# Kernel optimization log

Measured on AMD Instinct MI355X. Metric: run time of the kernel, lower is better.

Reference implementation:

```python
import jax, jax.numpy as jnp
from jax import lax
import numpy as np

V, K, T, E = 20000, 50, 50, 300   # vocab, topics, windows, rho_size
TH, EH, L, B = 800, 200, 3, 64    # t_hidden, eta_hidden, lstm layers, batch
DELTA = 0.005


def setup_inputs() -> dict:
    key = jax.random.key(0)
    ks = jax.random.split(key, 32)
    f32 = jnp.float32
    def nrm(i, shape, scale=1.0):
        return jax.random.normal(ks[i], shape, f32) * scale
    w = 0.02  # small init for linear weights so softplus/exp paths stay sane
    return {
        'bows': jax.random.uniform(ks[0], (B, V), f32),
        'normalized_bows': jax.random.uniform(ks[1], (B, V), f32),
        'times': jax.random.randint(ks[2], (B,), 0, T),
        'rnn_inp': jax.random.uniform(ks[3], (T, V), f32),
        'num_docs': 100000,
        'eps_alpha': nrm(4, (T, K, E)),
        'eps_eta': nrm(5, (T, K)),
        'eps_theta': nrm(6, (B, K)),
        'rho': nrm(7, (V, E), 0.1),
        'mu_q_alpha': nrm(8, (K, T, E), 0.1),
        'logsigma_q_alpha': nrm(9, (K, T, E), 0.1),
        'qtheta_W1': nrm(10, (TH, V + K), w), 'qtheta_b1': jnp.zeros((TH,), f32),
        'qtheta_W2': nrm(11, (TH, TH), w), 'qtheta_b2': jnp.zeros((TH,), f32),
        'mu_theta_W': nrm(12, (K, TH), w), 'mu_theta_b': jnp.zeros((K,), f32),
        'ls_theta_W': nrm(13, (K, TH), w), 'ls_theta_b': jnp.zeros((K,), f32),
        'eta_map_W': nrm(14, (EH, V), w), 'eta_map_b': jnp.zeros((EH,), f32),
        'lstm_Wih': nrm(15, (L, 4 * EH, EH), w), 'lstm_Whh': nrm(16, (L, 4 * EH, EH), w),
        'lstm_bih': jnp.zeros((L, 4 * EH), f32), 'lstm_bhh': jnp.zeros((L, 4 * EH), f32),
        'mu_eta_W': nrm(17, (K, EH + K), w), 'mu_eta_b': jnp.zeros((K,), f32),
        'ls_eta_W': nrm(18, (K, EH + K), w), 'ls_eta_b': jnp.zeros((K,), f32),
    }


def _kl(q_mu, q_ls, p_mu, p_ls):
    # KL(N(q_mu, e^{q_ls}) || N(p_mu, e^{p_ls})), summed over last dim (matches torch)
    return 0.5 * jnp.sum((jnp.exp(q_ls) + (q_mu - p_mu) ** 2) / (jnp.exp(p_ls) + 1e-6)
                         - 1.0 + p_ls - q_ls, axis=-1)


def _detm_forward(rho, mu_q_alpha, logsigma_q_alpha, qtheta_W1, qtheta_b1, qtheta_W2,
                  qtheta_b2, mu_theta_W, mu_theta_b, ls_theta_W, ls_theta_b, eta_map_W,
                  eta_map_b, lstm_Wih, lstm_Whh, lstm_bih, lstm_bhh, mu_eta_W, mu_eta_b,
                  ls_eta_W, ls_eta_b, bows, normalized_bows, rnn_inp, eps_alpha, eps_eta,
                  eps_theta, times):
    f32 = normalized_bows.dtype
    log_delta = jnp.log(jnp.asarray(DELTA, f32))
    zK = jnp.zeros((K,), f32)

    # ---- get_alpha (training): reparam is vectorizable; KL chains on alpha[t-1] ----
    mu_a = jnp.transpose(mu_q_alpha, (1, 0, 2))        # (T,K,E)
    ls_a = jnp.transpose(logsigma_q_alpha, (1, 0, 2))  # (T,K,E)
    alphas = mu_a + eps_alpha * jnp.exp(0.5 * ls_a)    # (T,K,E)
    kl_a0 = _kl(mu_a[0], ls_a[0], jnp.zeros_like(mu_a[0]), jnp.zeros_like(ls_a[0]))
    kl_at = _kl(mu_a[1:], ls_a[1:], alphas[:-1], log_delta)  # (T-1,K)
    kl_alpha = kl_a0.sum() + kl_at.sum()

    # ---- get_eta: q_eta_map -> 3-layer LSTM (batch 1) -> sequential eta chain ----
    x = rnn_inp @ eta_map_W.T + eta_map_b  # (T,EH)
    for l in range(L):
        Wih, Whh = lstm_Wih[l], lstm_Whh[l]
        bih, bhh = lstm_bih[l], lstm_bhh[l]
        def cell(carry, xt):
            h, c = carry
            g = Wih @ xt + bih + Whh @ h + bhh
            i, f, gg, o = jnp.split(g, 4)  # torch gate order: i, f, g, o
            c = jax.nn.sigmoid(f) * c + jax.nn.sigmoid(i) * jnp.tanh(gg)
            h = jax.nn.sigmoid(o) * jnp.tanh(c)
            return (h, c), h
        zH = jnp.zeros((EH,), f32)
        _, x = lax.scan(cell, (zH, zH), x)

    inp0 = jnp.concatenate([x[0], zK])
    mu0 = mu_eta_W @ inp0 + mu_eta_b
    ls0 = ls_eta_W @ inp0 + ls_eta_b
    eta0 = mu0 + eps_eta[0] * jnp.exp(0.5 * ls0)
    kl_e0 = _kl(mu0, ls0, zK, zK)

    def eta_step(eta_prev, xs):
        out_t, eps_t = xs
        inp = jnp.concatenate([out_t, eta_prev])
        mu = mu_eta_W @ inp + mu_eta_b
        ls = ls_eta_W @ inp + ls_eta_b
        eta = mu + eps_t * jnp.exp(0.5 * ls)
        kl = _kl(mu, ls, eta_prev, log_delta)
        return eta, (eta, kl)

    _, (etas_rest, kl_es) = lax.scan(eta_step, eta0, (x[1:], eps_eta[1:]))
    etas = jnp.concatenate([eta0[None], etas_rest], axis=0)  # (T,K)
    kl_eta = kl_e0 + kl_es.sum()

    # ---- get_theta ----
    eta_td = etas[times]  # (B,K)
    inp = jnp.concatenate([normalized_bows, eta_td], axis=1)  # (B, V+K)
    h = jax.nn.relu(inp @ qtheta_W1.T + qtheta_b1)
    h = jax.nn.relu(h @ qtheta_W2.T + qtheta_b2)
    mu_t = h @ mu_theta_W.T + mu_theta_b
    ls_t = h @ ls_theta_W.T + ls_theta_b
    z = mu_t + eps_theta * jnp.exp(0.5 * ls_t)
    theta = jax.nn.softmax(z, axis=-1)  # (B,K)
    kl_theta = _kl(mu_t, ls_t, eta_td, jnp.zeros_like(ls_t))  # (B,)

    # ---- get_beta + nll ----
    logit = jnp.einsum('tke,ve->tkv', alphas, rho)  # (T,K,V)
    beta = jax.nn.softmax(logit, axis=-1)
    beta_td = beta[times]  # (B,K,V)
    lik = jnp.einsum('bk,bkv->bv', theta, beta_td)
    nll_doc = -jnp.sum(jnp.log(lik + 1e-6) * normalized_bows, axis=-1)  # (B,)

    bsz = jnp.asarray(normalized_bows.shape[0], f32)
    nll = nll_doc.sum() / bsz
    kl_theta = kl_theta.sum() / bsz
    nelbo = nll + kl_alpha + kl_eta + kl_theta
    return nelbo, nll, kl_alpha, kl_eta, kl_theta


def reference(bows, normalized_bows, times, rnn_inp, num_docs, eps_alpha, eps_eta,
              eps_theta, rho, mu_q_alpha, logsigma_q_alpha, qtheta_W1, qtheta_b1,
              qtheta_W2, qtheta_b2, mu_theta_W, mu_theta_b, ls_theta_W, ls_theta_b,
              eta_map_W, eta_map_b, lstm_Wih, lstm_Whh, lstm_bih, lstm_bhh, mu_eta_W,
              mu_eta_b, ls_eta_W, ls_eta_b):
    # num_docs only feeds the unused `coeff` in the original forward
    return _detm_forward(rho, mu_q_alpha, logsigma_q_alpha, qtheta_W1, qtheta_b1,
                         qtheta_W2, qtheta_b2, mu_theta_W, mu_theta_b, ls_theta_W,
                         ls_theta_b, eta_map_W, eta_map_b, lstm_Wih, lstm_Whh,
                         lstm_bih, lstm_bhh, mu_eta_W, mu_eta_b, ls_eta_W, ls_eta_b,
                         bows, normalized_bows, rnn_inp, eps_alpha, eps_eta,
                         eps_theta, times)
```

## Files before the change

### kernel.cpp

```cpp
#include <hip/hip_runtime.h>
#include <math.h>

#define V_ 20000
#define K_ 50
#define T_ 50
#define E_ 300
#define TH_ 800
#define EH_ 200
#define B_ 64

#define WS_SC      0
#define WS_ALPHAS  8
#define WS_X0      750008
#define WS_X1      760008
#define WS_PRE     770008
#define WS_ETAS    810008
#define WS_H1      812508
#define WS_H2      863708
#define WS_THETA   914908
#define WS_M       918108
#define WS_S       920608
#define WS_PM      923108
#define WS_PS      1315608
#define WS_EPART   WS_PM
#define WS_TPRES   WS_PRE

#define SA 68
#define SNB 204
#define VC 512

__device__ __forceinline__ float sigf(float x){ return 1.0f/(1.0f+expf(-x)); }

__global__ void k_zero(float* ws){
  int i = blockIdx.x*256 + threadIdx.x;
  if (i < 8) ws[WS_SC + i] = 0.f;
  else if (i < 8 + 51200) ws[WS_H1 + (i-8)] = 0.f;
}

__global__ void __launch_bounds__(256) k_alpha(const float* mu_q, const float* ls_q,
                                               const float* eps, float* ws){
  int bid = blockIdx.x; int t = bid / K_, k = bid % K_;
  int tid = threadIdx.x;
  const float log_delta = logf(0.005f);
  const float pvar = expf(log_delta) + 1e-6f;
  float kl = 0.f;
  for (int e = tid; e < E_; e += 256){
    float mu = mu_q[(k*T_ + t)*E_ + e];
    float ls = ls_q[(k*T_ + t)*E_ + e];
    float ep = eps[(t*K_ + k)*E_ + e];
    float al = mu + ep*expf(0.5f*ls);
    ws[WS_ALPHAS + (t*K_ + k)*E_ + e] = al;
    if (t == 0){
      kl += 0.5f*((expf(ls) + mu*mu)/(1.f + 1e-6f) - 1.f - ls);
    } else {
      float mup = mu_q[(k*T_ + (t-1))*E_ + e];
      float lsp = ls_q[(k*T_ + (t-1))*E_ + e];
      float epp = eps[((t-1)*K_ + k)*E_ + e];
      float ap  = mup + epp*expf(0.5f*lsp);
      float d = mu - ap;
      kl += 0.5f*((expf(ls) + d*d)/pvar - 1.f + log_delta - ls);
    }
  }
  __shared__ float red[256];
  red[tid] = kl; __syncthreads();
  for (int s = 128; s; s >>= 1){ if (tid < s) red[tid] += red[tid+s]; __syncthreads(); }
  if (tid == 0) atomicAdd(&ws[WS_SC + 0], red[0]);
}

__global__ void __launch_bounds__(256) k_eta_gemm(const float* rnn, const float* W, float* ws){
  int vc = blockIdx.x;
  int h0 = blockIdx.y * 8;
  int t0 = blockIdx.z * 25;
  int v0 = vc * VC;
  int valid4 = (V_ - v0 >= VC) ? (VC >> 2) : ((V_ - v0) >> 2);
  int tid = threadIdx.x;
  __shared__ __align__(16) float rs[25*VC];
  for (int idx = tid; idx < 25*128; idx += 256){
    int r = idx >> 7, c = idx & 127;
    float4 v = (c < valid4) ? *(const float4*)&rnn[(size_t)(t0 + r)*V_ + v0 + 4*c]
                            : make_float4(0.f,0.f,0.f,0.f);
    *(float4*)&rs[r*VC + 4*c] = v;
  }
  int g = tid >> 5, lane = tid & 31;
  float4 wreg[4];
  #pragma unroll
  for (int i = 0; i < 4; ++i){
    int c4 = lane + 32*i;
    wreg[i] = (c4 < valid4) ? *(const float4*)&W[(size_t)(h0+g)*V_ + v0 + 4*c4]
                            : make_float4(0.f,0.f,0.f,0.f);
  }
  __syncthreads();
  for (int tl = 0; tl < 25; ++tl){
    const float* rrow = rs + tl*VC;
    float s = 0.f;
    #pragma unroll
    for (int i = 0; i < 4; ++i){
      float4 a = *(const float4*)&rrow[4*(lane + 32*i)];
      s += a.x*wreg[i].x + a.y*wreg[i].y + a.z*wreg[i].z + a.w*wreg[i].w;
    }
    #pragma unroll
    for (int m = 16; m; m >>= 1) s += __shfl_xor(s, m, 32);
    if (lane == 0) ws[WS_EPART + vc*(T_*EH_) + (t0 + tl)*EH_ + h0 + g] = s;
  }
}

__global__ void k_eta_merge(float* ws){
  int idx = blockIdx.x*256 + threadIdx.x;
  if (idx >= T_*EH_) return;
  float s = 0.f;
  for (int vc = 0; vc < 40; ++vc) s += ws[WS_EPART + vc*(T_*EH_) + idx];
  ws[WS_X0 + idx] = s;
}

__global__ void __launch_bounds__(832) k_lstm_pre(const float* Wih, const float* bih,
                                                  const float* bhh, const float* emb,
                                                  const float* xin, float* pre, int layer){
  int t = blockIdx.x, tid = threadIdx.x;
  __shared__ __align__(16) float xs[EH_];
  if (tid < EH_) xs[tid] = xin[t*EH_ + tid] + (emb ? emb[tid] : 0.f);
  __syncthreads();
  if (tid < 800){
    const float4* w4 = (const float4*)(Wih + (size_t)layer*160000 + (size_t)tid*200);
    const float4* x4 = (const float4*)xs;
    float a0 = 0.f, a1 = 0.f;
    #pragma unroll 5
    for (int c = 0; c < 50; c += 2){
      float4 w = w4[c],   x = x4[c];
      a0 += w.x*x.x + w.y*x.y + w.z*x.z + w.w*x.w;
      float4 w2 = w4[c+1], x2 = x4[c+1];
      a1 += w2.x*x2.x + w2.y*x2.y + w2.z*x2.z + w2.w*x2.w;
    }
    pre[t*800 + tid] = a0 + a1 + bih[layer*800 + tid] + bhh[layer*800 + tid];
  }
}

__global__ void __launch_bounds__(1024) k_lstm_scan(const float* Whh, const float* pre,
                                                    float* xout, int layer){
  int tid = threadIdx.x;
  __shared__ __align__(16) float hs[EH_];
  __shared__ float cs[EH_];
  __shared__ float gs[800];
  if (tid < EH_){ hs[tid] = 0.f; cs[tid] = 0.f; }
  __syncthreads();
  const float4* w4 = (const float4*)(Whh + (size_t)layer*160000 + (size_t)(tid < 800 ? tid : 0)*200);
  for (int t = 0; t < T_; ++t){
    if (tid < 800){
      const float4* h4 = (const float4*)hs;
      float a0 = 0.f, a1 = 0.f;
      #pragma unroll 5
      for (int c = 0; c < 50; c += 2){
        float4 w = w4[c],   h = h4[c];
        a0 += w.x*h.x + w.y*h.y + w.z*h.z + w.w*h.w;
        float4 w2 = w4[c+1], h2 = h4[c+1];
        a1 += w2.x*h2.x + w2.y*h2.y + w2.z*h2.z + w2.w*h2.w;
      }
      gs[tid] = pre[t*800 + tid] + a0 + a1;
    }
    __syncthreads();
    if (tid < EH_){
      float ig = sigf(gs[tid]);
      float fg = sigf(gs[200+tid]);
      float gg = tanhf(gs[400+tid]);
      float og = sigf(gs[600+tid]);
      float cc = fg*cs[tid] + ig*gg;
      cs[tid] = cc;
      float hh = og*tanhf(cc);
      hs[tid] = hh;
      xout[t*EH_ + tid] = hh;
    }
    __syncthreads();
  }
}

__global__ void __launch_bounds__(256) k_eta_chain(const float* x, const float* Wmu,
                                                   const float* bmu, const float* Wls,
                                                   const float* bls, const float* eps_eta,
                                                   float* ws){
  int tid = threadIdx.x;
  __shared__ float xs[EH_];
  __shared__ float etap[2][K_];
  __shared__ float kls[K_];
  const float log_delta = logf(0.005f);
  const float pvar = expf(log_delta) + 1e-6f;
  int j = tid >> 2, q = tid & 3;
  float klacc = 0.f;
  for (int t = 0; t < T_; ++t){
    if (tid < EH_) xs[tid] = x[t*EH_ + tid];
    __syncthreads();
    int rb = t & 1, wb = rb ^ 1;
    if (j < K_){
      float pm = 0.f, pl = 0.f;
      for (int c = q; c < 250; c += 4){
        float inp = (c < 200) ? xs[c] : ((t == 0) ? 0.f : etap[rb][c-200]);
        pm += Wmu[j*250 + c]*inp;
        pl += Wls[j*250 + c]*inp;
      }
      pm += __shfl_xor(pm, 1, 4); pm += __shfl_xor(pm, 2, 4);
      pl += __shfl_xor(pl, 1, 4); pl += __shfl_xor(pl, 2, 4);
      if (q == 0){
        float mu = pm + bmu[j], lsv = pl + bls[j];
        float klj;
        if (t == 0){
          klj = 0.5f*((expf(lsv) + mu*mu)/(1.f + 1e-6f) - 1.f - lsv);
        } else {
          float d = mu - etap[rb][j];
          klj = 0.5f*((expf(lsv) + d*d)/pvar - 1.f + log_delta - lsv);
        }
        float eta = mu + eps_eta[t*K_ + j]*expf(0.5f*lsv);
        etap[wb][j] = eta;
        kls[j] = klj;
        ws[WS_ETAS + t*K_ + j] = eta;
      }
    }
    __syncthreads();
    if (tid < 64){
      float v = (tid < K_) ? kls[tid] : 0.f;
      for (int m = 32; m; m >>= 1) v += __shfl_xor(v, m, 64);
      if (tid == 0) klacc += v;
    }
    __syncthreads();
  }
  if (tid == 0) ws[WS_SC + 1] = klacc;
}

__global__ void k_tmask(const int* times, float* ws){
  int t = threadIdx.x;
  if (t < T_){
    int p = 0;
    for (int b = 0; b < B_; ++b) p |= (times[b] == t) ? 1 : 0;
    ((int*)ws)[WS_TPRES + t] = p;
  }
}

__global__ void __launch_bounds__(256) k_h1_gemm(const float* nb, const float* W1, float* ws){
  int v0 = blockIdx.x * 2000;
  int r0 = blockIdx.y * 32;
  int tid = threadIdx.x;
  __shared__ __align__(16) float nbs[64*SNB];
  __shared__ __align__(16) float w1s[32*SNB];
  int dg = tid & 15, rg = tid >> 4;
  float acc[2][4] = {};
  for (int vs = 0; vs < 10; ++vs){
    int vbase = v0 + vs*200;
    __syncthreads();
    for (int idx = tid; idx < 64*50; idx += 256){
      int d = idx / 50, qq = idx % 50;
      float4 val = *(const float4*)&nb[(size_t)d*V_ + vbase + 4*qq];
      *(float4*)&nbs[d*SNB + 4*qq] = val;
    }
    for (int idx = tid; idx < 32*100; idx += 256){
      int r = idx / 100, qq = idx % 100;
      float2 val = *(const float2*)&W1[(size_t)(r0+r)*20050 + vbase + 2*qq];
      *(float2*)&w1s[r*SNB + 2*qq] = val;
    }
    __syncthreads();
    for (int v = 0; v < 200; ++v){
      float a0 = w1s[rg*SNB + v];
      float a1 = w1s[(rg+16)*SNB + v];
      #pragma unroll
      for (int jd = 0; jd < 4; ++jd){
        float bb = nbs[(dg + 16*jd)*SNB + v];
        acc[0][jd] += a0*bb;
        acc[1][jd] += a1*bb;
      }
    }
  }
  #pragma unroll
  for (int ir = 0; ir < 2; ++ir)
    #pragma unroll
    for (int jd = 0; jd < 4; ++jd)
      atomicAdd(&ws[WS_H1 + (dg + 16*jd)*TH_ + r0 + rg + 16*ir], acc[ir][jd]);
}

__global__ void k_h1_final(const float* W1, const float* b1, const int* times, float* ws){
  int idx = blockIdx.x*256 + threadIdx.x;
  if (idx >= B_*TH_) return;
  int b = idx / TH_, r = idx % TH_;
  const float* et = ws + WS_ETAS + times[b]*K_;
  const float* w  = W1 + (size_t)r*20050 + V_;
  float s = ws[WS_H1 + idx] + b1[r];
  for (int k = 0; k < K_; ++k) s += w[k]*et[k];
  ws[WS_H1 + idx] = fmaxf(s, 0.f);
}

__global__ void __launch_bounds__(256) k_h2(const float* W2, const float* b2, float* ws){
  int r0 = blockIdx.x * 64;
  int b  = blockIdx.y;
  int tid = threadIdx.x;
  __shared__ __align__(16) float h1s[TH_];
  __shared__ float part[4*68];
  for (int i = tid; i < TH_; i += 256) h1s[i] = ws[WS_H1 + b*TH_ + i];
  __syncthreads();
  int rl = tid & 63, p = tid >> 6;
  int r = r0 + rl;
  float acc = 0.f;
  if (r < TH_){
    const float4* w4 = (const float4*)(W2 + (size_t)r*TH_ + p*200);
    const float4* h4 = (const float4*)(h1s + p*200);
    #pragma unroll 5
    for (int c = 0; c < 50; ++c){
      float4 w = w4[c], h = h4[c];
      acc += w.x*h.x + w.y*h.y + w.z*h.z + w.w*h.w;
    }
  }
  part[p*68 + rl] = acc;
  __syncthreads();
  if (tid < 64 && r0 + tid < TH_){
    float s = part[tid] + part[68+tid] + part[136+tid] + part[204+tid] + b2[r0+tid];
    ws[WS_H2 + b*TH_ + r0 + tid] = fmaxf(s, 0.f);
  }
}

__global__ void __launch_bounds__(128) k_theta(const float* Wmu, const float* bmu,
                                               const float* Wls, const float* bls,
                                               const float* eps_th, const int* times, float* ws){
  int b = blockIdx.x, tid = threadIdx.x;
  __shared__ __align__(16) float h2s[TH_];
  __shared__ float mus[K_], lss[K_];
  for (int i = tid; i < TH_; i += 128) h2s[i] = ws[WS_H2 + b*TH_ + i];
  __syncthreads();
  if (tid < 100){
    int j = (tid < 50) ? tid : tid - 50;
    const float* Wr = (tid < 50) ? (Wmu + j*TH_) : (Wls + j*TH_);
    const float4* w4 = (const float4*)Wr;
    const float4* h4 = (const float4*)h2s;
    float a = 0.f;
    #pragma unroll 5
    for (int c = 0; c < 200; ++c){
      float4 w = w4[c], h = h4[c];
      a += w.x*h.x + w.y*h.y + w.z*h.z + w.w*h.w;
    }
    if (tid < 50) mus[j] = a + bmu[j]; else lss[j] = a + bls[j];
  }
  __syncthreads();
  if (tid < 64){
    int k = tid;
    bool ok = (k < K_);
    float mu  = ok ? mus[k] : 0.f;
    float lsv = ok ? lss[k] : 0.f;
    float etd = ok ? ws[WS_ETAS + times[b]*K_ + k] : 0.f;
    float z   = ok ? (mu + eps_th[b*K_ + k]*expf(0.5f*lsv)) : -1e30f;
    float m = z;
    for (int s = 32; s; s >>= 1) m = fmaxf(m, __shfl_xor(m, s, 64));
    float ez = ok ? expf(z - m) : 0.f;
    float ssum = ez;
    for (int s = 32; s; s >>= 1) ssum += __shfl_xor(ssum, s, 64);
    if (ok) ws[WS_THETA + b*K_ + k] = ez / ssum;
    float d = mu - etd;
    float kl = ok ? 0.5f*((expf(lsv) + d*d)/(1.f + 1e-6f) - 1.f - lsv) : 0.f;
    for (int s = 32; s; s >>= 1) kl += __shfl_xor(kl, s, 64);
    if (tid == 0) atomicAdd(&ws[WS_SC + 2], kl);
  }
}

__global__ void __launch_bounds__(256) k_logit_stats(const float* rho, float* ws){
  int ct = blockIdx.x, rt = blockIdx.y;
  int row0 = rt*64, col0 = ct*128;
  {
    const int* pres = (const int*)ws + WS_TPRES;
    int tA = row0 / K_;
    int tB = (row0 + 63) / K_; if (tB > T_-1) tB = T_-1;
    bool need = false;
    for (int tt = tA; tt <= tB; ++tt) need = need || (pres[tt] != 0);
    if (!need) return;
  }
  int tid = threadIdx.x;
  __shared__ __align__(16) float As[64*SA];
  __shared__ __align__(16) float Rs[128*SA];
  int colg = tid & 15, rowg = tid >> 4;
  float acc[4][8] = {};
  const float* alphas = ws + WS_ALPHAS;
  for (int ec = 0; ec < 5; ++ec){
    int e0 = ec*64;
    int esz4 = (ec == 4) ? 11 : 16;
    __syncthreads();
    for (int idx = tid; idx < 64*esz4; idx += 256){
      int r = idx / esz4, qq = idx % esz4;
      int row = row0 + r;
      float4 v = (row < T_*K_) ? *(const float4*)&alphas[(size_t)row*E_ + e0 + 4*qq]
                               : make_float4(0.f,0.f,0.f,0.f);
      *(float4*)&As[r*SA + 4*qq] = v;
    }
    for (int idx = tid; idx < 128*esz4; idx += 256){
      int c = idx / esz4, qq = idx % esz4;
      int col = col0 + c;
      float4 v = (col < V_) ? *(const float4*)&rho[(size_t)col*E_ + e0 + 4*qq]
                            : make_float4(0.f,0.f,0.f,0.f);
      *(float4*)&Rs[c*SA + 4*qq] = v;
    }
    __syncthreads();
    for (int q = 0; q < esz4; ++q){
      float4 av[4], bv[8];
      #pragma unroll
      for (int i = 0; i < 4; ++i) av[i] = *(const float4*)&As[(rowg + 16*i)*SA + 4*q];
      #pragma unroll
      for (int jj = 0; jj < 8; ++jj) bv[jj] = *(const float4*)&Rs[(colg + 16*jj)*SA + 4*q];
      #pragma unroll
      for (int i = 0; i < 4; ++i)
        #pragma unroll
        for (int jj = 0; jj < 8; ++jj)
          acc[i][jj] += av[i].x*bv[jj].x + av[i].y*bv[jj].y + av[i].z*bv[jj].z + av[i].w*bv[jj].w;
    }
  }
  #pragma unroll
  for (int i = 0; i < 4; ++i){
    int row = row0 + rowg + 16*i;
    float rm = -1e30f;
    #pragma unroll
    for (int jj = 0; jj < 8; ++jj){
      int col = col0 + colg + 16*jj;
      if (col < V_) rm = fmaxf(rm, acc[i][jj]);
    }
    for (int m = 1; m < 16; m <<= 1) rm = fmaxf(rm, __shfl_xor(rm, m, 16));
    float sm = 0.f;
    #pragma unroll
    for (int jj = 0; jj < 8; ++jj){
      int col = col0 + colg + 16*jj;
      if (col < V_) sm += expf(acc[i][jj] - rm);
    }
    for (int m = 1; m < 16; m <<= 1) sm += __shfl_xor(sm, m, 16);
    if (colg == 0 && row < T_*K_){
      ws[WS_PM + ct*2500 + row] = rm;
      ws[WS_PS + ct*2500 + row] = sm;
    }
  }
}

__global__ void k_stats_merge(float* ws){
  int row = blockIdx.x*8 + (threadIdx.x >> 5);
  int lane = threadIdx.x & 31;
  if (row >= T_*K_) return;
  float m = -1e30f;
  for (int i = lane; i < 157; i += 32) m = fmaxf(m, ws[WS_PM + i*2500 + row]);
  for (int s = 16; s; s >>= 1) m = fmaxf(m, __shfl_xor(m, s, 32));
  float ssum = 0.f;
  for (int i = lane; i < 157; i += 32)
    ssum += ws[WS_PS + i*2500 + row]*expf(ws[WS_PM + i*2500 + row] - m);
  for (int s = 16; s; s >>= 1) ssum += __shfl_xor(ssum, s, 32);
  if (lane == 0){ ws[WS_M + row] = m; ws[WS_S + row] = ssum; }
}

__global__ void __launch_bounds__(256) k_lik(const float* rho, const float* nb,
                                             const int* times, float* ws){
  int ct = blockIdx.x, t = blockIdx.y;
  int col0 = ct*64;
  int tid = threadIdx.x;
  __shared__ unsigned long long dmask;
  bool pred = (tid < B_) && (times[tid < B_ ? tid : 0] == t);
  unsigned long long mk = __ballot(pred);
  if (tid == 0) dmask = mk;
  __syncthreads();
  unsigned long long mask = dmask;
  if (mask == 0ull) return;

  __shared__ __align__(16) float As[64*SA];
  __shared__ __align__(16) float Rs[64*SA];
  __shared__ float P[50*SA];
  __shared__ float Qs[4*68];
  int colg = tid & 15, rowg = tid >> 4;
  float acc[4][4] = {};
  for (int ec = 0; ec < 5; ++ec){
    int e0 = ec*64;
    int esz4 = (ec == 4) ? 11 : 16;
    __syncthreads();
    for (int idx = tid; idx < 64*esz4; idx += 256){
      int r = idx / esz4, qq = idx % esz4;
      float4 v = (r < K_) ? *(const float4*)&ws[WS_ALPHAS + (size_t)(t*K_ + r)*E_ + e0 + 4*qq]
                          : make_float4(0.f,0.f,0.f,0.f);
      *(float4*)&As[r*SA + 4*qq] = v;
    }
    for (int idx = tid; idx < 64*esz4; idx += 256){
      int c = idx / esz4, qq = idx % esz4;
      int col = col0 + c;
      float4 v = (col < V_) ? *(const float4*)&rho[(size_t)col*E_ + e0 + 4*qq]
                            : make_float4(0.f,0.f,0.f,0.f);
      *(float4*)&Rs[c*SA + 4*qq] = v;
    }
    __syncthreads();
    for (int q = 0; q < esz4; ++q){
      float4 av[4], bv[4];
      #pragma unroll
      for (int i = 0; i < 4; ++i) av[i] = *(const float4*)&As[(rowg + 16*i)*SA + 4*q];
      #pragma unroll
      for (int jj = 0; jj < 4; ++jj) bv[jj] = *(const float4*)&Rs[(colg + 16*jj)*SA + 4*q];
      #pragma unroll
      for (int i = 0; i < 4; ++i)
        #pragma unroll
        for (int jj = 0; jj < 4; ++jj)
          acc[i][jj] += av[i].x*bv[jj].x + av[i].y*bv[jj].y + av[i].z*bv[jj].z + av[i].w*bv[jj].w;
    }
  }
  #pragma unroll
  for (int i = 0; i < 4; ++i){
    int r = rowg + 16*i;
    if (r < K_){
      float mm = ws[WS_M + t*K_ + r];
      float si = 1.f / ws[WS_S + t*K_ + r];
      #pragma unroll
      for (int jj = 0; jj < 4; ++jj){
        int col = col0 + colg + 16*jj;
        if (col < V_) P[r*SA + colg + 16*jj] = expf(acc[i][jj] - mm)*si;
      }
    }
  }
  __syncthreads();
  float nllloc = 0.f;
  int cl = tid & 63, kk = tid >> 6;
  for (unsigned long long m2 = mask; m2; m2 &= (m2-1)){
    int b = __ffsll((long long)m2) - 1;
    float partial = 0.f;
    for (int k = kk; k < K_; k += 4)
      partial += ws[WS_THETA + b*K_ + k]*P[k*SA + cl];
    Qs[kk*68 + cl] = partial;
    __syncthreads();
    if (tid < 64){
      float qv = Qs[cl] + Qs[68+cl] + Qs[136+cl] + Qs[204+cl];
      int col = col0 + cl;
      float term = (col < V_) ? (-logf(qv + 1e-6f)*nb[(size_t)b*V_ + col]) : 0.f;
      for (int s2 = 32; s2; s2 >>= 1) term += __shfl_xor(term, s2, 64);
      if (tid == 0) nllloc += term;
    }
    __syncthreads();
  }
  if (tid == 0) atomicAdd(&ws[WS_SC + 3], nllloc);
}

__global__ void k_final(const float* ws, float* out){
  if (threadIdx.x == 0 && blockIdx.x == 0){
    float nll = ws[WS_SC+3] / (float)B_;
    float kla = ws[WS_SC+0];
    float kle = ws[WS_SC+1];
    float klt = ws[WS_SC+2] / (float)B_;
    out[0] = nll + kla + kle + klt;
    out[1] = nll;
    out[2] = kla;
    out[3] = kle;
    out[4] = klt;
  }
}

extern "C" void kernel_launch(void* const* d_in, const int* in_sizes, int n_in,
                              void* d_out, int out_size, void* d_ws, size_t ws_size,
                              hipStream_t stream){
  const float* nb    = (const float*)d_in[1];
  const int*   times = (const int*)d_in[2];
  const float* rnn   = (const float*)d_in[3];
  const float* eps_a = (const float*)d_in[5];
  const float* eps_e = (const float*)d_in[6];
  const float* eps_t = (const float*)d_in[7];
  const float* rho   = (const float*)d_in[8];
  const float* mqa   = (const float*)d_in[9];
  const float* lqa   = (const float*)d_in[10];
  const float* W1    = (const float*)d_in[11];
  const float* b1    = (const float*)d_in[12];
  const float* W2    = (const float*)d_in[13];
  const float* b2    = (const float*)d_in[14];
  const float* Wmt   = (const float*)d_in[15];
  const float* bmt   = (const float*)d_in[16];
  const float* Wlt   = (const float*)d_in[17];
  const float* blt   = (const float*)d_in[18];
  const float* Wem   = (const float*)d_in[19];
  const float* bem   = (const float*)d_in[20];
  const float* Wih   = (const float*)d_in[21];
  const float* Whh   = (const float*)d_in[22];
  const float* bih   = (const float*)d_in[23];
  const float* bhh   = (const float*)d_in[24];
  const float* Wme   = (const float*)d_in[25];
  const float* bme   = (const float*)d_in[26];
  const float* Wle   = (const float*)d_in[27];
  const float* ble   = (const float*)d_in[28];
  float* ws  = (float*)d_ws;
  float* out = (float*)d_out;

  k_zero<<<dim3(201), dim3(256), 0, stream>>>(ws);
  k_alpha<<<dim3(2500), dim3(256), 0, stream>>>(mqa, lqa, eps_a, ws);
  k_eta_gemm<<<dim3(40,25,2), dim3(256), 0, stream>>>(rnn, Wem, ws);
  k_eta_merge<<<dim3(40), dim3(256), 0, stream>>>(ws);

  float* x0  = ws + WS_X0;
  float* x1  = ws + WS_X1;
  float* pre = ws + WS_PRE;
  k_lstm_pre<<<dim3(50), dim3(832), 0, stream>>>(Wih, bih, bhh, bem, x0, pre, 0);
  k_lstm_scan<<<dim3(1), dim3(1024), 0, stream>>>(Whh, pre, x1, 0);
  k_lstm_pre<<<dim3(50), dim3(832), 0, stream>>>(Wih, bih, bhh, (const float*)nullptr, x1, pre, 1);
  k_lstm_scan<<<dim3(1), dim3(1024), 0, stream>>>(Whh, pre, x0, 1);
  k_lstm_pre<<<dim3(50), dim3(832), 0, stream>>>(Wih, bih, bhh, (const float*)nullptr, x0, pre, 2);
  k_lstm_scan<<<dim3(1), dim3(1024), 0, stream>>>(Whh, pre, x1, 2);

  k_eta_chain<<<dim3(1), dim3(256), 0, stream>>>(x1, Wme, bme, Wle, ble, eps_e, ws);
  k_tmask<<<dim3(1), dim3(64), 0, stream>>>(times, ws);

  k_h1_gemm<<<dim3(10,25), dim3(256), 0, stream>>>(nb, W1, ws);
  k_h1_final<<<dim3(200), dim3(256), 0, stream>>>(W1, b1, times, ws);
  k_h2<<<dim3(13,64), dim3(256), 0, stream>>>(W2, b2, ws);
  k_theta<<<dim3(64), dim3(128), 0, stream>>>(Wmt, bmt, Wlt, blt, eps_t, times, ws);

  k_logit_stats<<<dim3(157,40), dim3(256), 0, stream>>>(rho, ws);
  k_stats_merge<<<dim3(313), dim3(256), 0, stream>>>(ws);
  k_lik<<<dim3(313,50), dim3(256), 0, stream>>>(rho, nb, times, ws);

  k_final<<<dim3(1), dim3(64), 0, stream>>>(ws, out);
}
```

Before: 4.064 ms.

## Use bf16 MFMA for logit-stats and likelihood GEMMs with larger tiles

Both rho-by-alpha GEMMs (the softmax statistics pass and the likelihood pass) drop their scalar fp32 FMA inner loops. Operands are converted to bf16 as they are staged into shared memory, and the products run on __builtin_amdgcn_mfma_f32_16x16x32_bf16 with a 2x2 wave layout. Tiles are enlarged: 128x128 for the statistics pass and 64x128 for the likelihood pass, with the grids adjusted to match and per-wave row max/sum partials merged in shared memory. This is meant to move the dominant matmul work onto matrix cores. The cost is bf16 rounding of the logits feeding a 20000-way softmax and log-likelihood.

```diff
diff --git a/kernel.cpp b/kernel.cpp
--- a/kernel.cpp
+++ b/kernel.cpp
@@ -25,11 +25,19 @@
 #define WS_EPART   WS_PM
 #define WS_TPRES   WS_PRE
 
-#define SA 68
 #define SNB 204
 #define VC 512
+#define SAB 104
+
+typedef short short8 __attribute__((ext_vector_type(8)));
+typedef float floatx4 __attribute__((ext_vector_type(4)));
 
 __device__ __forceinline__ float sigf(float x){ return 1.0f/(1.0f+expf(-x)); }
+
+__device__ __forceinline__ unsigned short f2bf(float f){
+  unsigned int u = __float_as_uint(f);
+  return (unsigned short)((u + 0x7FFFu + ((u >> 16) & 1u)) >> 16);
+}
 
 __global__ void k_zero(float* ws){
   int i = blockIdx.x*256 + threadIdx.x;
@@ -355,73 +363,110 @@
 
 __global__ void __launch_bounds__(256) k_logit_stats(const float* rho, float* ws){
   int ct = blockIdx.x, rt = blockIdx.y;
-  int row0 = rt*64, col0 = ct*128;
+  int row0 = rt*128, col0 = ct*128;
   {
     const int* pres = (const int*)ws + WS_TPRES;
     int tA = row0 / K_;
-    int tB = (row0 + 63) / K_; if (tB > T_-1) tB = T_-1;
+    int tB = (row0 + 127) / K_; if (tB > T_-1) tB = T_-1;
     bool need = false;
     for (int tt = tA; tt <= tB; ++tt) need = need || (pres[tt] != 0);
     if (!need) return;
   }
   int tid = threadIdx.x;
-  __shared__ __align__(16) float As[64*SA];
-  __shared__ __align__(16) float Rs[128*SA];
-  int colg = tid & 15, rowg = tid >> 4;
-  float acc[4][8] = {};
-  const float* alphas = ws + WS_ALPHAS;
-  for (int ec = 0; ec < 5; ++ec){
-    int e0 = ec*64;
-    int esz4 = (ec == 4) ? 11 : 16;
-    __syncthreads();
-    for (int idx = tid; idx < 64*esz4; idx += 256){
-      int r = idx / esz4, qq = idx % esz4;
+  __shared__ __align__(16) unsigned short As[128*SAB];
+  __shared__ __align__(16) unsigned short Rs[128*SAB];
+  __shared__ float pmw[2][128], psw[2][128];
+  int w = tid >> 6, lane = tid & 63;
+  int wr = w >> 1, wc = w & 1;
+  int l15 = lane & 15, l4 = lane >> 4;
+
+  floatx4 z4 = {0.f, 0.f, 0.f, 0.f};
+  floatx4 acc[4][4];
+  #pragma unroll
+  for (int i = 0; i < 4; ++i)
+    #pragma unroll
+    for (int j = 0; j < 4; ++j) acc[i][j] = z4;
+
+  for (int ec = 0; ec < 4; ++ec){
+    int kbase = ec*96;
+    int kvalid = (E_ - kbase < 96) ? (E_ - kbase) : 96;
+    int q4max = kvalid >> 2;
+    __syncthreads();
+    for (int idx = tid; idx < 128*26; idx += 256){
+      int r = idx / 26, q4 = idx % 26;
       int row = row0 + r;
-      float4 v = (row < T_*K_) ? *(const float4*)&alphas[(size_t)row*E_ + e0 + 4*qq]
-                               : make_float4(0.f,0.f,0.f,0.f);
-      *(float4*)&As[r*SA + 4*qq] = v;
-    }
-    for (int idx = tid; idx < 128*esz4; idx += 256){
-      int c = idx / esz4, qq = idx % esz4;
+      ushort4 o = {0,0,0,0};
+      if (q4 < q4max && row < T_*K_){
+        float4 v = *(const float4*)&ws[WS_ALPHAS + (size_t)row*E_ + kbase + 4*q4];
+        o.x = f2bf(v.x); o.y = f2bf(v.y); o.z = f2bf(v.z); o.w = f2bf(v.w);
+      }
+      *(ushort4*)&As[r*SAB + 4*q4] = o;
+    }
+    for (int idx = tid; idx < 128*26; idx += 256){
+      int c = idx / 26, q4 = idx % 26;
       int col = col0 + c;
-      float4 v = (col < V_) ? *(const float4*)&rho[(size_t)col*E_ + e0 + 4*qq]
-                            : make_float4(0.f,0.f,0.f,0.f);
-      *(float4*)&Rs[c*SA + 4*qq] = v;
-    }
-    __syncthreads();
-    for (int q = 0; q < esz4; ++q){
-      float4 av[4], bv[8];
-      #pragma unroll
-      for (int i = 0; i < 4; ++i) av[i] = *(const float4*)&As[(rowg + 16*i)*SA + 4*q];
-      #pragma unroll
-      for (int jj = 0; jj < 8; ++jj) bv[jj] = *(const float4*)&Rs[(colg + 16*jj)*SA + 4*q];
+      ushort4 o = {0,0,0,0};
+      if (q4 < q4max && col < V_){
+        float4 v = *(const float4*)&rho[(size_t)col*E_ + kbase + 4*q4];
+        o.x = f2bf(v.x); o.y = f2bf(v.y); o.z = f2bf(v.z); o.w = f2bf(v.w);
+      }
+      *(ushort4*)&Rs[c*SAB + 4*q4] = o;
+    }
+    __syncthreads();
+    int ksteps = (kvalid + 31) >> 5;
+    for (int ks = 0; ks < ksteps; ++ks){
+      int koff = ks*32 + l4*8;
+      short8 af[4], bf[4];
+      #pragma unroll
+      for (int i = 0; i < 4; ++i)
+        af[i] = *(const short8*)&As[(wr*64 + i*16 + l15)*SAB + koff];
+      #pragma unroll
+      for (int j = 0; j < 4; ++j)
+        bf[j] = *(const short8*)&Rs[(wc*64 + j*16 + l15)*SAB + koff];
       #pragma unroll
       for (int i = 0; i < 4; ++i)
         #pragma unroll
-        for (int jj = 0; jj < 8; ++jj)
-          acc[i][jj] += av[i].x*bv[jj].x + av[i].y*bv[jj].y + av[i].z*bv[jj].z + av[i].w*bv[jj].w;
+        for (int j = 0; j < 4; ++j)
+          acc[i][j] = __builtin_amdgcn_mfma_f32_16x16x32_bf16(af[i], bf[j], acc[i][j], 0, 0, 0);
     }
   }
   #pragma unroll
-  for (int i = 0; i < 4; ++i){
-    int row = row0 + rowg + 16*i;
-    float rm = -1e30f;
-    #pragma unroll
-    for (int jj = 0; jj < 8; ++jj){
-      int col = col0 + colg + 16*jj;
-      if (col < V_) rm = fmaxf(rm, acc[i][jj]);
-    }
-    for (int m = 1; m < 16; m <<= 1) rm = fmaxf(rm, __shfl_xor(rm, m, 16));
-    float sm = 0.f;
-    #pragma unroll
-    for (int jj = 0; jj < 8; ++jj){
-      int col = col0 + colg + 16*jj;
-      if (col < V_) sm += expf(acc[i][jj] - rm);
-    }
-    for (int m = 1; m < 16; m <<= 1) sm += __shfl_xor(sm, m, 16);
-    if (colg == 0 && row < T_*K_){
-      ws[WS_PM + ct*2500 + row] = rm;
-      ws[WS_PS + ct*2500 + row] = sm;
+  for (int rg = 0; rg < 4; ++rg){
+    #pragma unroll
+    for (int r = 0; r < 4; ++r){
+      float vmax = -1e30f;
+      #pragma unroll
+      for (int cf = 0; cf < 4; ++cf){
+        int col = col0 + wc*64 + cf*16 + l15;
+        if (col < V_) vmax = fmaxf(vmax, acc[rg][cf][r]);
+      }
+      vmax = fmaxf(vmax, __shfl_xor(vmax, 1, 64));
+      vmax = fmaxf(vmax, __shfl_xor(vmax, 2, 64));
+      vmax = fmaxf(vmax, __shfl_xor(vmax, 4, 64));
+      vmax = fmaxf(vmax, __shfl_xor(vmax, 8, 64));
+      float sx = 0.f;
+      #pragma unroll
+      for (int cf = 0; cf < 4; ++cf){
+        int col = col0 + wc*64 + cf*16 + l15;
+        if (col < V_) sx += expf(acc[rg][cf][r] - vmax);
+      }
+      sx += __shfl_xor(sx, 1, 64); sx += __shfl_xor(sx, 2, 64);
+      sx += __shfl_xor(sx, 4, 64); sx += __shfl_xor(sx, 8, 64);
+      if (l15 == 0){
+        int rl = wr*64 + rg*16 + l4*4 + r;
+        pmw[wc][rl] = vmax; psw[wc][rl] = sx;
+      }
+    }
+  }
+  __syncthreads();
+  if (tid < 128){
+    float m0 = pmw[0][tid], m1 = pmw[1][tid];
+    float mm = fmaxf(m0, m1);
+    float ss = psw[0][tid]*expf(m0 - mm) + psw[1][tid]*expf(m1 - mm);
+    int row = row0 + tid;
+    if (row < T_*K_){
+      ws[WS_PM + ct*2500 + row] = mm;
+      ws[WS_PS + ct*2500 + row] = ss;
     }
   }
 }
@@ -443,7 +488,7 @@
 __global__ void __launch_bounds__(256) k_lik(const float* rho, const float* nb,
                                              const int* times, float* ws){
   int ct = blockIdx.x, t = blockIdx.y;
-  int col0 = ct*64;
+  int col0 = ct*128;
   int tid = threadIdx.x;
   __shared__ unsigned long long dmask;
   bool pred = (tid < B_) && (times[tid < B_ ? tid : 0] == t);
@@ -453,73 +498,104 @@
   unsigned long long mask = dmask;
   if (mask == 0ull) return;
 
-  __shared__ __align__(16) float As[64*SA];
-  __shared__ __align__(16) float Rs[64*SA];
-  __shared__ float P[50*SA];
-  __shared__ float Qs[4*68];
-  int colg = tid & 15, rowg = tid >> 4;
-  float acc[4][4] = {};
-  for (int ec = 0; ec < 5; ++ec){
-    int e0 = ec*64;
-    int esz4 = (ec == 4) ? 11 : 16;
-    __syncthreads();
-    for (int idx = tid; idx < 64*esz4; idx += 256){
-      int r = idx / esz4, qq = idx % esz4;
-      float4 v = (r < K_) ? *(const float4*)&ws[WS_ALPHAS + (size_t)(t*K_ + r)*E_ + e0 + 4*qq]
-                          : make_float4(0.f,0.f,0.f,0.f);
-      *(float4*)&As[r*SA + 4*qq] = v;
-    }
-    for (int idx = tid; idx < 64*esz4; idx += 256){
-      int c = idx / esz4, qq = idx % esz4;
+  __shared__ __align__(16) char smem[64*SAB*2 + 128*SAB*2];
+  __shared__ float Qs[256];
+  __shared__ float red2[2];
+  unsigned short* As = (unsigned short*)smem;
+  unsigned short* Rs = (unsigned short*)(smem + 64*SAB*2);
+
+  int w = tid >> 6, lane = tid & 63;
+  int wr = w >> 1, wc = w & 1;
+  int l15 = lane & 15, l4 = lane >> 4;
+
+  floatx4 z4 = {0.f, 0.f, 0.f, 0.f};
+  floatx4 acc[2][4];
+  #pragma unroll
+  for (int i = 0; i < 2; ++i)
+    #pragma unroll
+    for (int j = 0; j < 4; ++j) acc[i][j] = z4;
+
+  for (int ec = 0; ec < 4; ++ec){
+    int kbase = ec*96;
+    int kvalid = (E_ - kbase < 96) ? (E_ - kbase) : 96;
+    int q4max = kvalid >> 2;
+    __syncthreads();
+    for (int idx = tid; idx < 64*26; idx += 256){
+      int r = idx / 26, q4 = idx % 26;
+      ushort4 o = {0,0,0,0};
+      if (q4 < q4max && r < K_){
+        float4 v = *(const float4*)&ws[WS_ALPHAS + (size_t)(t*K_ + r)*E_ + kbase + 4*q4];
+        o.x = f2bf(v.x); o.y = f2bf(v.y); o.z = f2bf(v.z); o.w = f2bf(v.w);
+      }
+      *(ushort4*)&As[r*SAB + 4*q4] = o;
+    }
+    for (int idx = tid; idx < 128*26; idx += 256){
+      int c = idx / 26, q4 = idx % 26;
       int col = col0 + c;
-      float4 v = (col < V_) ? *(const float4*)&rho[(size_t)col*E_ + e0 + 4*qq]
-                            : make_float4(0.f,0.f,0.f,0.f);
-      *(float4*)&Rs[c*SA + 4*qq] = v;
-    }
-    __syncthreads();
-    for (int q = 0; q < esz4; ++q){
-      float4 av[4], bv[4];
-      #pragma unroll
-      for (int i = 0; i < 4; ++i) av[i] = *(const float4*)&As[(rowg + 16*i)*SA + 4*q];
-      #pragma unroll
-      for (int jj = 0; jj < 4; ++jj) bv[jj] = *(const float4*)&Rs[(colg + 16*jj)*SA + 4*q];
-      #pragma unroll
-      for (int i = 0; i < 4; ++i)
+      ushort4 o = {0,0,0,0};
+      if (q4 < q4max && col < V_){
+        float4 v = *(const float4*)&rho[(size_t)col*E_ + kbase + 4*q4];
+        o.x = f2bf(v.x); o.y = f2bf(v.y); o.z = f2bf(v.z); o.w = f2bf(v.w);
+      }
+      *(ushort4*)&Rs[c*SAB + 4*q4] = o;
+    }
+    __syncthreads();
+    int ksteps = (kvalid + 31) >> 5;
+    for (int ks = 0; ks < ksteps; ++ks){
+      int koff = ks*32 + l4*8;
+      short8 af[2], bf[4];
+      #pragma unroll
+      for (int i = 0; i < 2; ++i)
+        af[i] = *(const short8*)&As[(wr*32 + i*16 + l15)*SAB + koff];
+      #pragma unroll
+      for (int j = 0; j < 4; ++j)
+        bf[j] = *(const short8*)&Rs[(wc*64 + j*16 + l15)*SAB + koff];
+      #pragma unroll
+      for (int i = 0; i < 2; ++i)
         #pragma unroll
-        for (int jj = 0; jj < 4; ++jj)
-          acc[i][jj] += av[i].x*bv[jj].x + av[i].y*bv[jj].y + av[i].z*bv[jj].z + av[i].w*bv[jj].w;
-    }
-  }
+        for (int j = 0; j < 4; ++j)
+          acc[i][j] = __builtin_amdgcn_mfma_f32_16x16x32_bf16(af[i], bf[j], acc[i][j], 0, 0, 0);
+    }
+  }
+  __syncthreads();
+  float* P = (float*)smem;
   #pragma unroll
-  for (int i = 0; i < 4; ++i){
-    int r = rowg + 16*i;
-    if (r < K_){
-      float mm = ws[WS_M + t*K_ + r];
-      float si = 1.f / ws[WS_S + t*K_ + r];
-      #pragma unroll
-      for (int jj = 0; jj < 4; ++jj){
-        int col = col0 + colg + 16*jj;
-        if (col < V_) P[r*SA + colg + 16*jj] = expf(acc[i][jj] - mm)*si;
+  for (int rg = 0; rg < 2; ++rg){
+    #pragma unroll
+    for (int r = 0; r < 4; ++r){
+      int rl = wr*32 + rg*16 + l4*4 + r;
+      if (rl < K_){
+        float mm = ws[WS_M + t*K_ + rl];
+        float si = 1.f / ws[WS_S + t*K_ + rl];
+        #pragma unroll
+        for (int cf = 0; cf < 4; ++cf){
+          int cl = wc*64 + cf*16 + l15;
+          if (col0 + cl < V_) P[rl*136 + cl] = expf(acc[rg][cf][r] - mm)*si;
+        }
       }
     }
   }
   __syncthreads();
   float nllloc = 0.f;
-  int cl = tid & 63, kk = tid >> 6;
+  int cl = tid & 127, kk = tid >> 7;
   for (unsigned long long m2 = mask; m2; m2 &= (m2-1)){
     int b = __ffsll((long long)m2) - 1;
     float partial = 0.f;
-    for (int k = kk; k < K_; k += 4)
-      partial += ws[WS_THETA + b*K_ + k]*P[k*SA + cl];
-    Qs[kk*68 + cl] = partial;
-    __syncthreads();
-    if (tid < 64){
-      float qv = Qs[cl] + Qs[68+cl] + Qs[136+cl] + Qs[204+cl];
-      int col = col0 + cl;
-      float term = (col < V_) ? (-logf(qv + 1e-6f)*nb[(size_t)b*V_ + col]) : 0.f;
+    #pragma unroll
+    for (int k = 0; k < 25; ++k)
+      partial += ws[WS_THETA + b*K_ + kk*25 + k] * P[(kk*25 + k)*136 + cl];
+    Qs[kk*128 + cl] = partial;
+    __syncthreads();
+    if (tid < 128){
+      float q = Qs[tid] + Qs[128 + tid];
+      int col = col0 + tid;
+      float term = (col < V_) ? (-logf(q + 1e-6f)*nb[(size_t)b*V_ + col]) : 0.f;
+      #pragma unroll
       for (int s2 = 32; s2; s2 >>= 1) term += __shfl_xor(term, s2, 64);
-      if (tid == 0) nllloc += term;
-    }
+      if ((tid & 63) == 0) red2[tid >> 6] = term;
+    }
+    __syncthreads();
+    if (tid == 0) nllloc += red2[0] + red2[1];
     __syncthreads();
   }
   if (tid == 0) atomicAdd(&ws[WS_SC + 3], nllloc);
@@ -595,9 +671,9 @@
   k_h2<<<dim3(13,64), dim3(256), 0, stream>>>(W2, b2, ws);
   k_theta<<<dim3(64), dim3(128), 0, stream>>>(Wmt, bmt, Wlt, blt, eps_t, times, ws);
 
-  k_logit_stats<<<dim3(157,40), dim3(256), 0, stream>>>(rho, ws);
+  k_logit_stats<<<dim3(157,20), dim3(256), 0, stream>>>(rho, ws);
   k_stats_merge<<<dim3(313), dim3(256), 0, stream>>>(ws);
-  k_lik<<<dim3(313,50), dim3(256), 0, stream>>>(rho, nb, times, ws);
+  k_lik<<<dim3(157,50), dim3(256), 0, stream>>>(rho, nb, times, ws);
 
   k_final<<<dim3(1), dim3(64), 0, stream>>>(ws, out);
 }
```

Result: faster. 3.440 ms (-15.4%).
